# Performance work log

Measured on AMD Instinct MI355X. Metric: run time of the kernel, lower is better.

## Reference

```python
import jax, jax.numpy as jnp
import numpy as np

EMB_LEN = 16384
EMB_DIM = 128
BETA = 0.25
WEIGHT_DECAY = 0.01


def resize_linear(x, axis, out_size):
    # PyTorch (tri)linear interpolation, align_corners=False, separable per axis.
    in_size = x.shape[axis]
    if in_size == out_size:
        return x
    src = (jnp.arange(out_size, dtype=jnp.float32) + 0.5) * (in_size / out_size) - 0.5
    src = jnp.clip(src, 0.0, in_size - 1.0)
    i0 = jnp.floor(src).astype(jnp.int32)
    i1 = jnp.minimum(i0 + 1, in_size - 1)
    w1 = src - i0.astype(jnp.float32)
    x0 = jnp.take(x, i0, axis=axis)
    x1 = jnp.take(x, i1, axis=axis)
    bshape = [1] * x.ndim
    bshape[axis] = out_size
    w1 = w1.reshape(bshape)
    return x0 * (1.0 - w1) + x1 * w1


def setup_inputs() -> dict:
    key = jax.random.key(0)
    k1, k2 = jax.random.split(key)
    b, c, h, w = 16384, 16, 2, 4  # h*w must equal 8 (see shape analysis)
    z = jax.random.normal(k1, (b, c, h, w), dtype=jnp.float32)
    emb_weight = jax.random.uniform(
        k2, (EMB_LEN, EMB_DIM), dtype=jnp.float32,
        minval=-1.0 / EMB_LEN, maxval=1.0 / EMB_LEN)
    return {"z": z, "emb_weight": emb_weight}


def reference(z, emb_weight):
    b, c, h, w = z.shape
    # feature_unfolding: F.interpolate(x, 2, mode='trilinear') -> size=(2,2,2)
    x = z[:, :, None, :, :]                       # [b,c,1,h,w]
    x = resize_linear(x, 2, 2)                    # depth 1 -> 2 (duplicate)
    x = resize_linear(x, 3, 2)                    # h -> 2
    x = resize_linear(x, 4, 2)                    # w -> 2
    # pixelshuffle3D_downscale(scale=2) on [b,c,2,2,2] -> [b,8c,1,1,1];
    # flatten order matches contiguous reshape.
    zf = x.reshape(b, c * 8)                      # [b, emb_dim]
    # squared L2 distance via expansion
    d = (jnp.sum(zf ** 2, axis=1, keepdims=True)
         + jnp.sum(emb_weight ** 2, axis=1)
         - 2.0 * zf @ emb_weight.T)               # [b, emb_len]
    idx = jnp.argmin(d, axis=1)                   # [b]
    z_q = emb_weight[idx].reshape(b, c, h, w)
    sg = jax.lax.stop_gradient
    commit = BETA * jnp.mean((sg(z_q) - z) ** 2) + jnp.mean((z_q - sg(z)) ** 2)
    zd = sg(z)
    vx = z_q - jnp.mean(z_q)
    vy = zd - jnp.mean(zd)
    pearson = 0.5 + 0.5 * jnp.sum(vx * vy) / (
        jnp.sqrt(jnp.sum(vx ** 2)) * jnp.sqrt(jnp.sum(vy ** 2)))
    # torch.linalg.norm(W, ord=1) on 2D matrix = max column abs-sum
    reg = WEIGHT_DECAY * jnp.max(jnp.sum(jnp.abs(emb_weight), axis=0))
    loss = commit + pearson + reg
    z_q_out = z + sg(z_q - z)                     # straight-through
    # rearrange 'b h w c -> b c h w' on a [b,c,h,w] tensor == permute(0,3,1,2)
    z_q_out = jnp.transpose(z_q_out, (0, 3, 1, 2))
    return z_q_out, loss, idx
```

## Files before the change

### kernel.cpp

```cpp
#include <hip/hip_runtime.h>
#include <cstdint>
#include <cstddef>

#define B_ROWS 16384
#define EMB_LEN 16384
#define K_DIM 128
#define JSPLIT 8
#define JLEN (EMB_LEN / JSPLIT)
#define RB 32
#define JT 256
#define KC 16

typedef const __attribute__((address_space(1))) void* gas_vp;
typedef __attribute__((address_space(3))) void* las_vp;

__device__ __forceinline__ void dma16(const float* g, float* l) {
    __builtin_amdgcn_global_load_lds((gas_vp)g, (las_vp)l, 16, 0, 0);
}

__global__ void zf_kernel(const float* __restrict__ z,
                          float* __restrict__ zf, float* __restrict__ Cb) {
    int b = blockIdx.x;
    int i = threadIdx.x;
    int c = i >> 3, h = (i >> 1) & 1, wp = i & 1;
    const float* zr = z + (size_t)b * 128 + c * 8 + h * 4 + wp * 2;
    float v = 0.5f * zr[0] + 0.5f * zr[1];
    zf[(size_t)b * 128 + i] = v;
    float s = v * v;
    for (int o = 32; o; o >>= 1) s += __shfl_down(s, o, 64);
    __shared__ float sm[2];
    if ((threadIdx.x & 63) == 0) sm[threadIdx.x >> 6] = s;
    __syncthreads();
    if (threadIdx.x == 0) Cb[b] = sm[0] + sm[1];
}

__global__ void transpose_kernel(const float* __restrict__ emb,
                                 float* __restrict__ embT) {
    __shared__ float t[128][65];
    int j0 = blockIdx.x * 64;
    int jl = threadIdx.x >> 2;
    int kq = threadIdx.x & 3;
    const float* er = emb + (size_t)(j0 + jl) * 128;
#pragma unroll
    for (int q = 0; q < 8; ++q) {
        int k4 = (kq * 8 + q) * 4;
        float4 v = *(const float4*)(er + k4);
        t[k4 + 0][jl] = v.x;
        t[k4 + 1][jl] = v.y;
        t[k4 + 2][jl] = v.z;
        t[k4 + 3][jl] = v.w;
    }
    __syncthreads();
    int kk = threadIdx.x >> 4;
    int jl4 = (threadIdx.x & 15) * 4;
#pragma unroll
    for (int q = 0; q < 8; ++q) {
        int k = kk + q * 16;
        float4 v = make_float4(t[k][jl4], t[k][jl4 + 1], t[k][jl4 + 2], t[k][jl4 + 3]);
        *(float4*)(embT + (size_t)k * EMB_LEN + j0 + jl4) = v;
    }
}

#define FMA_ROW(cr, av) \
    cr.x = fmaf(av, bv.x, cr.x); \
    cr.y = fmaf(av, bv.y, cr.y); \
    cr.z = fmaf(av, bv.z, cr.z); \
    cr.w = fmaf(av, bv.w, cr.w);

#define EPI(rr, cr) { \
    float cbr = cbs[w8 + rr]; \
    float bd = cbr - 2.0f * cr.x; int bj = jb; \
    float dv = cbr - 2.0f * cr.y; if (dv < bd) { bd = dv; bj = jb + 1; } \
    dv = cbr - 2.0f * cr.z; if (dv < bd) { bd = dv; bj = jb + 2; } \
    dv = cbr - 2.0f * cr.w; if (dv < bd) { bd = dv; bj = jb + 3; } \
    for (int o = 32; o; o >>= 1) { \
        float d2 = __shfl_down(bd, o, 64); \
        int j2 = __shfl_down(bj, o, 64); \
        if (d2 < bd || (d2 == bd && j2 < bj)) { bd = d2; bj = j2; } \
    } \
    if (l == 0 && bd < bwd[w8 + rr]) { bwd[w8 + rr] = bd; bwj[w8 + rr] = bj; } \
}

__global__ void argmin_kernel(const float* __restrict__ zf,
                              const float* __restrict__ Cb,
                              const float* __restrict__ embT,
                              float* __restrict__ cand_d,
                              int* __restrict__ cand_j) {
    __shared__ float zfs[K_DIM][RB + 4];
    __shared__ float es[KC][JT];
    __shared__ float cbs[RB];
    __shared__ float bwd[RB];
    __shared__ int   bwj[RB];

    int sp = blockIdx.x & 7;
    int rb = blockIdx.x >> 3;
    int rbase = rb * RB;
    int jbase = sp * JLEN;
    int tid = threadIdx.x;
    int w = tid >> 6;
    int l = tid & 63;
    int w8 = w << 3;
    int l4 = l << 2;

    {
        int r0 = tid >> 3;
        int kq0 = tid & 7;
        const float* zr = zf + (size_t)(rbase + r0) * K_DIM;
        for (int kq = kq0; kq < 32; kq += 8) {
            float4 v = *(const float4*)(zr + kq * 4);
            zfs[kq * 4 + 0][r0] = v.x;
            zfs[kq * 4 + 1][r0] = v.y;
            zfs[kq * 4 + 2][r0] = v.z;
            zfs[kq * 4 + 3][r0] = v.w;
        }
        if (tid < RB) {
            cbs[tid] = Cb[rbase + tid];
            bwd[tid] = 3.4e38f;
            bwj[tid] = 0;
        }
    }

    for (int jt = 0; jt < JLEN; jt += JT) {
        float4 c0 = make_float4(0.f, 0.f, 0.f, 0.f);
        float4 c1 = make_float4(0.f, 0.f, 0.f, 0.f);
        float4 c2 = make_float4(0.f, 0.f, 0.f, 0.f);
        float4 c3 = make_float4(0.f, 0.f, 0.f, 0.f);
        float4 c4 = make_float4(0.f, 0.f, 0.f, 0.f);
        float4 c5 = make_float4(0.f, 0.f, 0.f, 0.f);
        float4 c6 = make_float4(0.f, 0.f, 0.f, 0.f);
        float4 c7 = make_float4(0.f, 0.f, 0.f, 0.f);

        for (int kc = 0; kc < K_DIM; kc += KC) {
            __syncthreads();
            {
                const float* gb = embT + (size_t)kc * EMB_LEN + jbase + jt + l4;
                float* lb = &es[w][0];
                dma16(gb + (size_t)(0 + w) * EMB_LEN, lb + 0 * JT);
                dma16(gb + (size_t)(4 + w) * EMB_LEN, lb + 4 * JT);
                dma16(gb + (size_t)(8 + w) * EMB_LEN, lb + 8 * JT);
                dma16(gb + (size_t)(12 + w) * EMB_LEN, lb + 12 * JT);
            }
            __syncthreads();

#pragma unroll
            for (int k = 0; k < KC; ++k) {
                const float4 a0 = *(const float4*)(&zfs[kc + k][w8]);
                const float4 a1 = *(const float4*)(&zfs[kc + k][w8 + 4]);
                const float4 bv = *(const float4*)(&es[k][l4]);
                FMA_ROW(c0, a0.x)
                FMA_ROW(c1, a0.y)
                FMA_ROW(c2, a0.z)
                FMA_ROW(c3, a0.w)
                FMA_ROW(c4, a1.x)
                FMA_ROW(c5, a1.y)
                FMA_ROW(c6, a1.z)
                FMA_ROW(c7, a1.w)
            }
        }

        int jb = jbase + jt + l4;
        EPI(0, c0)
        EPI(1, c1)
        EPI(2, c2)
        EPI(3, c3)
        EPI(4, c4)
        EPI(5, c5)
        EPI(6, c6)
        EPI(7, c7)
    }

    __syncthreads();
    if (tid < RB) {
        cand_d[sp * B_ROWS + rbase + tid] = bwd[tid];
        cand_j[sp * B_ROWS + rbase + tid] = bwj[tid];
    }
}

__global__ void merge_kernel(const float* __restrict__ cand_d,
                             const int* __restrict__ cand_j,
                             int* __restrict__ idxw,
                             float* __restrict__ out_idx) {
    int b = blockIdx.x * 256 + threadIdx.x;
    float bd = cand_d[b];
    int bj = cand_j[b];
#pragma unroll
    for (int s = 1; s < JSPLIT; ++s) {
        float d = cand_d[s * B_ROWS + b];
        int j = cand_j[s * B_ROWS + b];
        if (d < bd) { bd = d; bj = j; }
    }
    idxw[b] = bj;
    out_idx[b] = (float)bj;
}

__global__ void output_kernel(const float* __restrict__ z,
                              const float* __restrict__ emb,
                              const int* __restrict__ idxw,
                              float* __restrict__ out,
                              double* __restrict__ accs) {
    int stride = gridDim.x * blockDim.x;
    double s[6] = {0, 0, 0, 0, 0, 0};
    for (int n = blockIdx.x * blockDim.x + threadIdx.x; n < B_ROWS * 128; n += stride) {
        int b = n >> 7, i = n & 127;
        int c = i >> 3, h = (i >> 2) & 1, w = i & 3;
        float zv = z[n];
        float qv = emb[(size_t)idxw[b] * 128 + i];
        float diff = qv - zv;
        out[(size_t)((b * 4 + w) * 16 + c) * 2 + h] = zv + diff;
        s[0] += (double)qv;
        s[1] += (double)zv;
        s[2] += (double)qv * qv;
        s[3] += (double)zv * zv;
        s[4] += (double)qv * zv;
        s[5] += (double)diff * diff;
    }
    int lane = threadIdx.x & 63, wv = threadIdx.x >> 6;
#pragma unroll
    for (int q = 0; q < 6; ++q)
        for (int o = 32; o; o >>= 1) s[q] += __shfl_down(s[q], o, 64);
    __shared__ double sm[6][4];
    if (lane == 0)
#pragma unroll
        for (int q = 0; q < 6; ++q) sm[q][wv] = s[q];
    __syncthreads();
    if (threadIdx.x == 0) {
#pragma unroll
        for (int q = 0; q < 6; ++q)
            atomicAdd(&accs[q], sm[q][0] + sm[q][1] + sm[q][2] + sm[q][3]);
    }
}

__global__ void colsum_kernel(const float* __restrict__ emb, float* __restrict__ colsum) {
    int j = blockIdx.x;
    double s = 0;
    for (int i = threadIdx.x; i < EMB_LEN; i += blockDim.x)
        s += (double)fabsf(emb[(size_t)i * 128 + j]);
    int lane = threadIdx.x & 63, wv = threadIdx.x >> 6;
    for (int o = 32; o; o >>= 1) s += __shfl_down(s, o, 64);
    __shared__ double sm[4];
    if (lane == 0) sm[wv] = s;
    __syncthreads();
    if (threadIdx.x == 0) colsum[j] = (float)(sm[0] + sm[1] + sm[2] + sm[3]);
}

__global__ void loss_kernel(const double* __restrict__ accs,
                            const float* __restrict__ colsum,
                            float* __restrict__ out_loss) {
    __shared__ float sm[128];
    int tid = threadIdx.x;
    sm[tid] = colsum[tid];
    __syncthreads();
    for (int s = 64; s; s >>= 1) {
        if (tid < s) sm[tid] = fmaxf(sm[tid], sm[tid + s]);
        __syncthreads();
    }
    if (tid == 0) {
        double n = (double)B_ROWS * 128.0;
        double m = accs[5] / n;
        double commit = 0.25 * m + m;
        double Sx = accs[0], Sy = accs[1], Sxx = accs[2], Syy = accs[3], Sxy = accs[4];
        double cov = Sxy - Sx * Sy / n;
        double vx = Sxx - Sx * Sx / n;
        double vy = Syy - Sy * Sy / n;
        double pearson = 0.5 + 0.5 * cov / (sqrt(vx) * sqrt(vy));
        double reg = 0.01 * (double)sm[0];
        out_loss[0] = (float)(commit + pearson + reg);
    }
}

extern "C" void kernel_launch(void* const* d_in, const int* in_sizes, int n_in,
                              void* d_out, int out_size, void* d_ws, size_t ws_size,
                              hipStream_t stream) {
    const float* z = (const float*)d_in[0];
    const float* emb = (const float*)d_in[1];
    float* out = (float*)d_out;

    float* zf = (float*)d_ws;
    float* embT = zf + 2097152;
    float* Cb = embT + 2097152;
    float* cand_d = Cb + 16384;
    int* cand_j = (int*)(cand_d + JSPLIT * B_ROWS);
    int* idxw = cand_j + JSPLIT * B_ROWS;
    double* accs = (double*)(idxw + 16384);
    float* colsum = (float*)(accs + 8);

    hipMemsetAsync(accs, 0, 8 * sizeof(double), stream);

    zf_kernel<<<B_ROWS, 128, 0, stream>>>(z, zf, Cb);
    transpose_kernel<<<EMB_LEN / 64, 256, 0, stream>>>(emb, embT);
    argmin_kernel<<<512 * JSPLIT, 256, 0, stream>>>(zf, Cb, embT, cand_d, cand_j);
    merge_kernel<<<B_ROWS / 256, 256, 0, stream>>>(cand_d, cand_j, idxw, out + 2097153);
    output_kernel<<<1024, 256, 0, stream>>>(z, emb, idxw, out, accs);
    colsum_kernel<<<128, 256, 0, stream>>>(emb, colsum);
    loss_kernel<<<1, 128, 0, stream>>>(accs, colsum, out + 2097152);
}
```

Before: 1.047 ms.

## Double-buffer embedding tiles and defer argmin wave reduction to kernel end

```diff
diff --git a/kernel.cpp b/kernel.cpp
--- a/kernel.cpp
+++ b/kernel.cpp
@@ -67,18 +67,28 @@
     cr.z = fmaf(av, bv.z, cr.z); \
     cr.w = fmaf(av, bv.w, cr.w);
 
-#define EPI(rr, cr) { \
-    float cbr = cbs[w8 + rr]; \
-    float bd = cbr - 2.0f * cr.x; int bj = jb; \
-    float dv = cbr - 2.0f * cr.y; if (dv < bd) { bd = dv; bj = jb + 1; } \
-    dv = cbr - 2.0f * cr.z; if (dv < bd) { bd = dv; bj = jb + 2; } \
-    dv = cbr - 2.0f * cr.w; if (dv < bd) { bd = dv; bj = jb + 3; } \
+#define UPD(rr, cr) { \
+    float dv0 = cb##rr - 2.0f * cr.x; \
+    float dv1 = cb##rr - 2.0f * cr.y; \
+    float dv2 = cb##rr - 2.0f * cr.z; \
+    float dv3 = cb##rr - 2.0f * cr.w; \
+    if (dv0 < bd##rr) { bd##rr = dv0; bj##rr = jb; } \
+    if (dv1 < bd##rr) { bd##rr = dv1; bj##rr = jb + 1; } \
+    if (dv2 < bd##rr) { bd##rr = dv2; bj##rr = jb + 2; } \
+    if (dv3 < bd##rr) { bd##rr = dv3; bj##rr = jb + 3; } \
+}
+
+#define RED(rr) { \
+    float bd = bd##rr; int bj = bj##rr; \
     for (int o = 32; o; o >>= 1) { \
         float d2 = __shfl_down(bd, o, 64); \
         int j2 = __shfl_down(bj, o, 64); \
         if (d2 < bd || (d2 == bd && j2 < bj)) { bd = d2; bj = j2; } \
     } \
-    if (l == 0 && bd < bwd[w8 + rr]) { bwd[w8 + rr] = bd; bwj[w8 + rr] = bj; } \
+    if (l == 0) { \
+        cand_d[sp * B_ROWS + rbase + w8 + rr] = bd; \
+        cand_j[sp * B_ROWS + rbase + w8 + rr] = bj; \
+    } \
 }
 
 __global__ void argmin_kernel(const float* __restrict__ zf,
@@ -87,10 +97,7 @@
                               float* __restrict__ cand_d,
                               int* __restrict__ cand_j) {
     __shared__ float zfs[K_DIM][RB + 4];
-    __shared__ float es[KC][JT];
-    __shared__ float cbs[RB];
-    __shared__ float bwd[RB];
-    __shared__ int   bwj[RB];
+    __shared__ float es[2][KC][JT];
 
     int sp = blockIdx.x & 7;
     int rb = blockIdx.x >> 3;
@@ -113,13 +120,26 @@
             zfs[kq * 4 + 2][r0] = v.z;
             zfs[kq * 4 + 3][r0] = v.w;
         }
-        if (tid < RB) {
-            cbs[tid] = Cb[rbase + tid];
-            bwd[tid] = 3.4e38f;
-            bwj[tid] = 0;
-        }
-    }
-
+    }
+
+    const float* cbp = Cb + rbase + w8;
+    float cb0 = cbp[0], cb1 = cbp[1], cb2 = cbp[2], cb3 = cbp[3];
+    float cb4 = cbp[4], cb5 = cbp[5], cb6 = cbp[6], cb7 = cbp[7];
+
+    float bd0 = 3.4e38f, bd1 = 3.4e38f, bd2 = 3.4e38f, bd3 = 3.4e38f;
+    float bd4 = 3.4e38f, bd5 = 3.4e38f, bd6 = 3.4e38f, bd7 = 3.4e38f;
+    int bj0 = 0, bj1 = 0, bj2 = 0, bj3 = 0, bj4 = 0, bj5 = 0, bj6 = 0, bj7 = 0;
+
+    {
+        const float* gb = embT + jbase + l4;
+        float* lb = &es[0][w][0];
+        dma16(gb + (size_t)(0 + w) * EMB_LEN, lb + 0 * JT);
+        dma16(gb + (size_t)(4 + w) * EMB_LEN, lb + 4 * JT);
+        dma16(gb + (size_t)(8 + w) * EMB_LEN, lb + 8 * JT);
+        dma16(gb + (size_t)(12 + w) * EMB_LEN, lb + 12 * JT);
+    }
+
+    int buf = 0;
     for (int jt = 0; jt < JLEN; jt += JT) {
         float4 c0 = make_float4(0.f, 0.f, 0.f, 0.f);
         float4 c1 = make_float4(0.f, 0.f, 0.f, 0.f);
@@ -132,21 +152,26 @@
 
         for (int kc = 0; kc < K_DIM; kc += KC) {
             __syncthreads();
+
             {
-                const float* gb = embT + (size_t)kc * EMB_LEN + jbase + jt + l4;
-                float* lb = &es[w][0];
-                dma16(gb + (size_t)(0 + w) * EMB_LEN, lb + 0 * JT);
-                dma16(gb + (size_t)(4 + w) * EMB_LEN, lb + 4 * JT);
-                dma16(gb + (size_t)(8 + w) * EMB_LEN, lb + 8 * JT);
-                dma16(gb + (size_t)(12 + w) * EMB_LEN, lb + 12 * JT);
+                int kc2 = kc + KC, jt2 = jt;
+                if (kc2 == K_DIM) { kc2 = 0; jt2 += JT; }
+                if (jt2 < JLEN) {
+                    const float* gb = embT + (size_t)kc2 * EMB_LEN + jbase + jt2 + l4;
+                    float* lb = &es[buf ^ 1][w][0];
+                    dma16(gb + (size_t)(0 + w) * EMB_LEN, lb + 0 * JT);
+                    dma16(gb + (size_t)(4 + w) * EMB_LEN, lb + 4 * JT);
+                    dma16(gb + (size_t)(8 + w) * EMB_LEN, lb + 8 * JT);
+                    dma16(gb + (size_t)(12 + w) * EMB_LEN, lb + 12 * JT);
+                }
             }
-            __syncthreads();
-
+
+            const float (*eb)[JT] = es[buf];
 #pragma unroll
             for (int k = 0; k < KC; ++k) {
+                const float4 bv = *(const float4*)(&eb[k][l4]);
                 const float4 a0 = *(const float4*)(&zfs[kc + k][w8]);
                 const float4 a1 = *(const float4*)(&zfs[kc + k][w8 + 4]);
-                const float4 bv = *(const float4*)(&es[k][l4]);
                 FMA_ROW(c0, a0.x)
                 FMA_ROW(c1, a0.y)
                 FMA_ROW(c2, a0.z)
@@ -156,24 +181,28 @@
                 FMA_ROW(c6, a1.z)
                 FMA_ROW(c7, a1.w)
             }
+            buf ^= 1;
         }
 
         int jb = jbase + jt + l4;
-        EPI(0, c0)
-        EPI(1, c1)
-        EPI(2, c2)
-        EPI(3, c3)
-        EPI(4, c4)
-        EPI(5, c5)
-        EPI(6, c6)
-        EPI(7, c7)
-    }
-
-    __syncthreads();
-    if (tid < RB) {
-        cand_d[sp * B_ROWS + rbase + tid] = bwd[tid];
-        cand_j[sp * B_ROWS + rbase + tid] = bwj[tid];
-    }
+        UPD(0, c0)
+        UPD(1, c1)
+        UPD(2, c2)
+        UPD(3, c3)
+        UPD(4, c4)
+        UPD(5, c5)
+        UPD(6, c6)
+        UPD(7, c7)
+    }
+
+    RED(0)
+    RED(1)
+    RED(2)
+    RED(3)
+    RED(4)
+    RED(5)
+    RED(6)
+    RED(7)
 }
 
 __global__ void merge_kernel(const float* __restrict__ cand_d,
```

Result: faster. 990.7 us (-5.4%).
